# Performance work log

Measured on AMD Instinct MI355X. Metric: run time of the kernel, lower is better.

The kernel has to match this reference:

```python
import jax, jax.numpy as jnp
import numpy as np

N_NODES = 50000
NEG_SLOPE = 0.2


def _gat_conv(x, src, dst, W, a_src, a_dst, b, num_nodes):
    # W: [H*C, F_in]; a_src/a_dst: [H, C]; b: [H*C]
    H, C = a_src.shape
    xp = (x @ W.T).reshape(num_nodes, H, C)              # [N,H,C]
    alpha_s = jnp.sum(xp * a_src[None], axis=-1)          # [N,H]
    alpha_d = jnp.sum(xp * a_dst[None], axis=-1)          # [N,H]
    e = jax.nn.leaky_relu(alpha_s[src] + alpha_d[dst], NEG_SLOPE)  # [E,H]
    # segment softmax over incoming edges of each dst node (self-loops guarantee non-empty segments)
    m = jax.ops.segment_max(e, dst, num_segments=num_nodes)
    e = jnp.exp(e - m[dst])
    s = jax.ops.segment_sum(e, dst, num_segments=num_nodes)
    alpha = e / s[dst]                                    # [E,H]
    out = jax.ops.segment_sum(alpha[:, :, None] * xp[src], dst, num_segments=num_nodes)  # [N,H,C]
    return out.reshape(num_nodes, H * C) + b


def setup_inputs() -> dict:
    key = jax.random.key(0)
    ks = jax.random.split(key, 12)
    N, E, F_in, HID, H, Z = N_NODES, 800000, 128, 64, 2, 32
    sc = 0.1
    return {
        "features": jax.random.normal(ks[0], (N, F_in), jnp.float32),
        "edges": jax.random.randint(ks[1], (2, E), 0, N, jnp.int32),
        "W1": jax.random.normal(ks[2], (H * HID, F_in), jnp.float32) * sc,
        "a_src1": jax.random.normal(ks[3], (H, HID), jnp.float32) * sc,
        "a_dst1": jax.random.normal(ks[4], (H, HID), jnp.float32) * sc,
        "b1": jnp.zeros((H * HID,), jnp.float32),
        "W_mu": jax.random.normal(ks[5], (Z, H * HID), jnp.float32) * sc,
        "a_src_mu": jax.random.normal(ks[6], (1, Z), jnp.float32) * sc,
        "a_dst_mu": jax.random.normal(ks[7], (1, Z), jnp.float32) * sc,
        "b_mu": jnp.zeros((Z,), jnp.float32),
        "W_std": jax.random.normal(ks[8], (Z, H * HID), jnp.float32) * sc,
        "a_src_std": jax.random.normal(ks[9], (1, Z), jnp.float32) * sc,
        "a_dst_std": jax.random.normal(ks[10], (1, Z), jnp.float32) * sc,
        "b_std": jnp.zeros((Z,), jnp.float32),
    }


def reference(features, edges, W1, a_src1, a_dst1, b1, W_mu, a_src_mu, a_dst_mu, b_mu, W_std, a_src_std, a_dst_std, b_std):
    N = features.shape[0]
    loops = jnp.arange(N, dtype=edges.dtype)
    src = jnp.concatenate([edges[0], loops])  # add self loops (PyG default)
    dst = jnp.concatenate([edges[1], loops])
    h = _gat_conv(features, src, dst, W1, a_src1, a_dst1, b1, N)
    h = jax.nn.relu(h)  # dropout p=0.0 -> identity
    mu = _gat_conv(h, src, dst, W_mu, a_src_mu, a_dst_mu, b_mu, N)
    std = _gat_conv(h, src, dst, W_std, a_src_std, a_dst_std, b_std, N)
    return (mu, std)
```

## Files before the change

### kernel.cpp

```cpp
#include <hip/hip_runtime.h>
#include <math.h>

#define N_NODES 50000
#define N_EDGES 800000
#define ET (N_EDGES + N_NODES)
#define KD 128
#define Z 32
#define SH 7
#define BW 128
#define NBUCK ((N_NODES + BW - 1) / BW)
#define CHUNK 4096
#define NBLKA ((ET + CHUNK - 1) / CHUNK)
#define MTOT (NBUCK * NBLKA)
#define MBS ((MTOT + 1023) / 1024)

typedef __attribute__((ext_vector_type(8))) short bf16x8;
typedef __attribute__((ext_vector_type(4))) float f32x4;

static __device__ __forceinline__ float lrelu(float x){ return x > 0.f ? x : 0.2f*x; }
static __device__ __forceinline__ float bf2f(unsigned int u16){ return __uint_as_float(u16 << 16); }
static __device__ __forceinline__ float lof(unsigned int u){ return __uint_as_float(u << 16); }
static __device__ __forceinline__ float hif(unsigned int u){ return __uint_as_float(u & 0xffff0000u); }
static __device__ __forceinline__ unsigned short f2bf(float f){
  unsigned int x = __float_as_uint(f);
  return (unsigned short)((x + 0x7fffu + ((x >> 16) & 1u)) >> 16);
}

__global__ __launch_bounds__(256) void bhistA_kernel(const int* __restrict__ edges, int* __restrict__ M){
  int k = blockIdx.x, t = threadIdx.x;
  __shared__ int cnt[NBUCK];
  for(int b = t; b < NBUCK; b += 256) cnt[b] = 0;
  __syncthreads();
  int base = k*CHUNK;
  int lim = min(base + CHUNK, ET);
  for(int i = base + t; i < lim; i += 256){
    int d = (i < N_EDGES) ? edges[N_EDGES + i] : (i - N_EDGES);
    atomicAdd(&cnt[d >> SH], 1);
  }
  __syncthreads();
  for(int b = t; b < NBUCK; b += 256) M[b*NBLKA + k] = cnt[b];
}

__global__ __launch_bounds__(256) void scanM1_kernel(const int* __restrict__ M, int* __restrict__ bsumM){
  int b = blockIdx.x, t = threadIdx.x;
  int base = b*1024 + t*4;
  int s = 0;
  #pragma unroll
  for(int i=0;i<4;i++){ int n = base+i; if(n < MTOT) s += M[n]; }
  for(int off=32; off; off>>=1) s += __shfl_xor(s, off);
  __shared__ int ws[4];
  if((t&63)==0) ws[t>>6] = s;
  __syncthreads();
  if(t==0) bsumM[b] = ws[0]+ws[1]+ws[2]+ws[3];
}

__global__ __launch_bounds__(256) void scanM2_kernel(const int* __restrict__ bsumM, int* __restrict__ bpreM){
  __shared__ int sm[256];
  int t = threadIdx.x;
  int v = (t < MBS) ? bsumM[t] : 0;
  sm[t] = v;
  __syncthreads();
  for(int off=1; off<256; off<<=1){
    int u = (t >= off) ? sm[t-off] : 0;
    __syncthreads();
    sm[t] += u;
    __syncthreads();
  }
  if(t < MBS) bpreM[t] = sm[t] - v;
}

__global__ __launch_bounds__(256) void scanM3_kernel(const int* __restrict__ M, const int* __restrict__ bpreM,
                                                     int* __restrict__ Mpos){
  int b = blockIdx.x, t = threadIdx.x;
  int lane = t & 63, wv = t >> 6;
  int base = b*1024 + t*4;
  int d[4]; int s = 0;
  #pragma unroll
  for(int i=0;i<4;i++){ int n = base+i; d[i] = (n < MTOT) ? M[n] : 0; s += d[i]; }
  int v = s;
  for(int off=1; off<64; off<<=1){
    int u = __shfl_up(v, off);
    if(lane >= off) v += u;
  }
  int texcl = v - s;
  __shared__ int wtot[4];
  if(lane == 63) wtot[wv] = v;
  __syncthreads();
  int woff = 0;
  for(int i=0;i<wv;i++) woff += wtot[i];
  int run = bpreM[b] + woff + texcl;
  #pragma unroll
  for(int i=0;i<4;i++){
    int n = base+i;
    if(n < MTOT){ Mpos[n] = run; run += d[i]; }
  }
}

__global__ __launch_bounds__(256) void bplaceA_kernel(const int* __restrict__ edges, const int* __restrict__ Mpos,
                                                      int2* __restrict__ etmp){
  int k = blockIdx.x, t = threadIdx.x;
  __shared__ int cur[NBUCK];
  for(int b = t; b < NBUCK; b += 256) cur[b] = Mpos[b*NBLKA + k];
  __syncthreads();
  int base = k*CHUNK;
  int lim = min(base + CHUNK, ET);
  for(int i = base + t; i < lim; i += 256){
    int s, d;
    if(i < N_EDGES){ s = edges[i]; d = edges[N_EDGES+i]; } else { s = d = i - N_EDGES; }
    int pos = atomicAdd(&cur[d >> SH], 1);
    etmp[pos] = make_int2(s, d);
  }
}

__global__ __launch_bounds__(256) void bfin_kernel(const int* __restrict__ Mpos, const int2* __restrict__ etmp,
                                                   int* __restrict__ rowptr, int* __restrict__ esrc,
                                                   int* __restrict__ edst){
  int b = blockIdx.x, t = threadIdx.x;
  __shared__ int cnt[BW];
  __shared__ int pre[BW];
  __shared__ int lcur[BW];
  if(t < BW) cnt[t] = 0;
  __syncthreads();
  int beg = Mpos[b*NBLKA];
  int end = (b+1 < NBUCK) ? Mpos[(b+1)*NBLKA] : ET;
  for(int i = beg + t; i < end; i += 256) atomicAdd(&cnt[etmp[i].y & (BW-1)], 1);
  __syncthreads();
  if(t < BW) pre[t] = cnt[t];
  __syncthreads();
  for(int off=1; off<BW; off<<=1){
    int u = 0;
    if(t < BW && t >= off) u = pre[t-off];
    __syncthreads();
    if(t < BW) pre[t] += u;
    __syncthreads();
  }
  if(t < BW){
    int excl = pre[t] - cnt[t];
    int node = b*BW + t;
    if(node < N_NODES) rowptr[node] = beg + excl;
    lcur[t] = beg + excl;
  }
  if(b == 0 && t == 255) rowptr[N_NODES] = ET;
  __syncthreads();
  for(int i = beg + t; i < end; i += 256){
    int2 e = etmp[i];
    int pos = atomicAdd(&lcur[e.y & (BW-1)], 1);
    esrc[pos] = e.x;
    edst[pos] = e.y;
  }
}

__global__ __launch_bounds__(256) void wconv_kernel(const float* __restrict__ W1,
                                                    const float* __restrict__ Wmu, const float* __restrict__ Wst,
                                                    unsigned short* __restrict__ Wb1, unsigned short* __restrict__ Wb2){
  int i = blockIdx.x*256 + threadIdx.x;
  if(i < 128*KD) Wb1[i] = f2bf(W1[i]);
  if(i < 64*KD) Wb2[i] = f2bf(i < 32*KD ? Wmu[i] : Wst[i - 32*KD]);
}

__global__ __launch_bounds__(256) void mmt1_kernel(const float* __restrict__ X,
                                                   const unsigned short* __restrict__ Wb,
                                                   const float* __restrict__ asv, const float* __restrict__ adv,
                                                   unsigned short* __restrict__ outb,
                                                   float* __restrict__ as1, float* __restrict__ ad1){
  constexpr int OC = 128, CT = 8;
  int t = threadIdx.x;
  int w = t >> 6, L = t & 63;
  int col = L & 15, quad = L >> 4;
  int row0 = blockIdx.x*64 + w*16;
  int rA = row0 + col;
  if(rA >= N_NODES) rA = N_NODES-1;

  f32x4 acc[CT];
  #pragma unroll
  for(int ct=0;ct<CT;ct++) acc[ct] = (f32x4){0.f,0.f,0.f,0.f};

  #pragma unroll
  for(int kc=0;kc<4;kc++){
    int k0 = kc*32 + quad*8;
    const float* Xf = X + (size_t)rA*KD + k0;
    float4 p = *(const float4*)Xf;
    float4 q = *(const float4*)(Xf + 4);
    bf16x8 a;
    a[0] = (short)f2bf(p.x); a[1] = (short)f2bf(p.y);
    a[2] = (short)f2bf(p.z); a[3] = (short)f2bf(p.w);
    a[4] = (short)f2bf(q.x); a[5] = (short)f2bf(q.y);
    a[6] = (short)f2bf(q.z); a[7] = (short)f2bf(q.w);
    #pragma unroll
    for(int ct=0;ct<CT;ct++){
      bf16x8 b = *(const bf16x8*)(Wb + (size_t)(ct*16 + col)*KD + k0);
      acc[ct] = __builtin_amdgcn_mfma_f32_16x16x32_bf16(a, b, acc[ct], 0, 0, 0);
    }
  }

  float av[CT], dv[CT];
  #pragma unroll
  for(int ct=0;ct<CT;ct++){ av[ct] = asv[ct*16 + col]; dv[ct] = adv[ct*16 + col]; }

  #pragma unroll
  for(int r=0;r<4;r++){
    int row = row0 + quad*4 + r;
    #pragma unroll
    for(int ct=0;ct<CT;ct++)
      if(row < N_NODES) outb[(size_t)row*OC + ct*16 + col] = f2bf(acc[ct][r]);
    float s0 = acc[0][r]*av[0] + acc[1][r]*av[1] + acc[2][r]*av[2] + acc[3][r]*av[3];
    float s1 = acc[4][r]*av[4] + acc[5][r]*av[5] + acc[6][r]*av[6] + acc[7][r]*av[7];
    float d0 = acc[0][r]*dv[0] + acc[1][r]*dv[1] + acc[2][r]*dv[2] + acc[3][r]*dv[3];
    float d1 = acc[4][r]*dv[4] + acc[5][r]*dv[5] + acc[6][r]*dv[6] + acc[7][r]*dv[7];
    #pragma unroll
    for(int off=1; off<16; off<<=1){
      s0 += __shfl_xor(s0, off); s1 += __shfl_xor(s1, off);
      d0 += __shfl_xor(d0, off); d1 += __shfl_xor(d1, off);
    }
    if(col == 0 && row < N_NODES){
      as1[row*2] = s0; as1[row*2+1] = s1;
      ad1[row*2] = d0; ad1[row*2+1] = d1;
    }
  }
}

__global__ __launch_bounds__(256) void mmt2_kernel(const unsigned short* __restrict__ Xb,
                                                   const unsigned short* __restrict__ Wb,
                                                   const float* __restrict__ asmu, const float* __restrict__ admu,
                                                   const float* __restrict__ asst, const float* __restrict__ adst,
                                                   unsigned short* __restrict__ outb,
                                                   float* __restrict__ as2, float* __restrict__ ad2){
  constexpr int OC = 64, CT = 4;
  int t = threadIdx.x;
  int w = t >> 6, L = t & 63;
  int col = L & 15, quad = L >> 4;
  int row0 = blockIdx.x*64 + w*16;
  int rA = row0 + col;
  if(rA >= N_NODES) rA = N_NODES-1;

  f32x4 acc[CT];
  #pragma unroll
  for(int ct=0;ct<CT;ct++) acc[ct] = (f32x4){0.f,0.f,0.f,0.f};

  #pragma unroll
  for(int kc=0;kc<4;kc++){
    int k0 = kc*32 + quad*8;
    bf16x8 a = *(const bf16x8*)(Xb + (size_t)rA*KD + k0);
    #pragma unroll
    for(int ct=0;ct<CT;ct++){
      bf16x8 b = *(const bf16x8*)(Wb + (size_t)(ct*16 + col)*KD + k0);
      acc[ct] = __builtin_amdgcn_mfma_f32_16x16x32_bf16(a, b, acc[ct], 0, 0, 0);
    }
  }

  float av[CT], dv[CT];
  #pragma unroll
  for(int ct=0;ct<CT;ct++){
    av[ct] = (ct < 2) ? asmu[ct*16 + col] : asst[(ct-2)*16 + col];
    dv[ct] = (ct < 2) ? admu[ct*16 + col] : adst[(ct-2)*16 + col];
  }

  #pragma unroll
  for(int r=0;r<4;r++){
    int row = row0 + quad*4 + r;
    #pragma unroll
    for(int ct=0;ct<CT;ct++)
      if(row < N_NODES) outb[(size_t)row*OC + ct*16 + col] = f2bf(acc[ct][r]);
    float smu = acc[0][r]*av[0] + acc[1][r]*av[1];
    float sst = acc[2][r]*av[2] + acc[3][r]*av[3];
    float dmu = acc[0][r]*dv[0] + acc[1][r]*dv[1];
    float dst = acc[2][r]*dv[2] + acc[3][r]*dv[3];
    #pragma unroll
    for(int off=1; off<16; off<<=1){
      smu += __shfl_xor(smu, off); sst += __shfl_xor(sst, off);
      dmu += __shfl_xor(dmu, off); dst += __shfl_xor(dst, off);
    }
    if(col == 0 && row < N_NODES){
      as2[row*2] = smu; as2[row*2+1] = sst;
      ad2[row*2] = dmu; ad2[row*2+1] = dst;
    }
  }
}

__global__ __launch_bounds__(256) void wcalc_kernel(const int* __restrict__ esrc, const int* __restrict__ edst,
                                                    const float* __restrict__ as, const float* __restrict__ ad,
                                                    float2* __restrict__ wp){
  int i = blockIdx.x*256 + threadIdx.x;
  if(i >= ET) return;
  int s = esrc[i], d = edst[i];
  float2 a = ((const float2*)as)[s];
  float2 b = ((const float2*)ad)[d];
  wp[i] = make_float2(__expf(lrelu(a.x + b.x)), __expf(lrelu(a.y + b.y)));
}

__global__ __launch_bounds__(256) void agg1_kernel(const int* __restrict__ rowptr, const int* __restrict__ esrc,
                                                   const float2* __restrict__ wp,
                                                   const unsigned int* __restrict__ xb,
                                                   const float* __restrict__ b1, unsigned int* __restrict__ hb){
  int node = blockIdx.x*4 + (threadIdx.x>>6);
  int l = threadIdx.x & 63;
  if(node >= N_NODES) return;
  int beg = rowptr[node], end = rowptr[node+1];
  float accx = 0.f, accy = 0.f, s0 = 0.f, s1 = 0.f;
  int n = end - beg;
  int nq = n & ~7;

#define F1_E(j)  int e##j = esrc[i+j];
#define F1_W(j)  float2 w##j = wp[i+j];
#define F1_U(j)  unsigned int u##j = xb[(size_t)e##j*64 + l];
#define F1_C(j)  { s0 += w##j.x; s1 += w##j.y; \
                   float vv = (l < 32) ? w##j.x : w##j.y; \
                   accx += vv * lof(u##j); accy += vv * hif(u##j); }

  for(int i = beg; i < beg + nq; i += 8){
    F1_E(0) F1_E(1) F1_E(2) F1_E(3) F1_E(4) F1_E(5) F1_E(6) F1_E(7)
    F1_W(0) F1_W(1) F1_W(2) F1_W(3) F1_W(4) F1_W(5) F1_W(6) F1_W(7)
    F1_U(0) F1_U(1) F1_U(2) F1_U(3) F1_U(4) F1_U(5) F1_U(6) F1_U(7)
    F1_C(0) F1_C(1) F1_C(2) F1_C(3) F1_C(4) F1_C(5) F1_C(6) F1_C(7)
  }
  for(int i = beg + nq; i < end; i++){
    F1_E(0) F1_W(0) F1_U(0) F1_C(0)
  }
#undef F1_E
#undef F1_W
#undef F1_U
#undef F1_C
  float sd = (l < 32) ? s0 : s1;
  float2 bb = ((const float2*)b1)[l];
  float rx = fmaxf(accx/sd + bb.x, 0.f);
  float ry = fmaxf(accy/sd + bb.y, 0.f);
  unsigned int hp = (unsigned int)f2bf(rx) | ((unsigned int)f2bf(ry) << 16);
  hb[(size_t)node*64 + l] = hp;
}

__global__ __launch_bounds__(256) void agg2_kernel(const int* __restrict__ rowptr, const int* __restrict__ esrc,
                                                   const float2* __restrict__ wp,
                                                   const uint2* __restrict__ xb2,
                                                   const float* __restrict__ bmu, const float* __restrict__ bst,
                                                   float* __restrict__ out){
  int node = blockIdx.x*4 + (threadIdx.x>>6);
  int l = threadIdx.x & 63;
  if(node >= N_NODES) return;
  int g = l >> 4, c = l & 15;
  int beg = rowptr[node], end = rowptr[node+1];
  int n = end - beg;
  float a0=0.f, a1=0.f, a2=0.f, a3=0.f, smu=0.f, sst=0.f;
  int nquad = n >> 2;
  int mainq = nquad & ~3;

#define G2(j) int e##j = esrc[base + 4*j]; float2 w##j = wp[base + 4*j];
#define U2(j) uint2 u##j = xb2[(size_t)e##j*16 + c];
#define C2(j) { smu += w##j.x; sst += w##j.y; \
                float vv = (c < 8) ? w##j.x : w##j.y; \
                a0 += vv*lof(u##j.x); a1 += vv*hif(u##j.x); \
                a2 += vv*lof(u##j.y); a3 += vv*hif(u##j.y); }

  for(int qq = 0; qq < mainq; qq += 4){
    int base = beg + 4*qq + g;
    G2(0) G2(1) G2(2) G2(3)
    U2(0) U2(1) U2(2) U2(3)
    C2(0) C2(1) C2(2) C2(3)
  }
  for(int qq = mainq; qq < nquad; qq++){
    int base = beg + 4*qq + g;
    G2(0) U2(0) C2(0)
  }
  int tail = n & 3;
  if(g < tail){
    int idx = beg + 4*nquad + g;
    int e = esrc[idx];
    float2 w = wp[idx];
    uint2 u = xb2[(size_t)e*16 + c];
    smu += w.x; sst += w.y;
    float vv = (c < 8) ? w.x : w.y;
    a0 += vv*lof(u.x); a1 += vv*hif(u.x);
    a2 += vv*lof(u.y); a3 += vv*hif(u.y);
  }
#undef G2
#undef U2
#undef C2
  #pragma unroll
  for(int off = 16; off < 64; off <<= 1){
    smu += __shfl_xor(smu, off); sst += __shfl_xor(sst, off);
    a0 += __shfl_xor(a0, off); a1 += __shfl_xor(a1, off);
    a2 += __shfl_xor(a2, off); a3 += __shfl_xor(a3, off);
  }
  float sd = (c < 8) ? smu : sst;
  float4 bb = (c < 8) ? *(const float4*)(bmu + 4*c) : *(const float4*)(bst + 4*(c-8));
  float4 r;
  r.x = a0/sd + bb.x;
  r.y = a1/sd + bb.y;
  r.z = a2/sd + bb.z;
  r.w = a3/sd + bb.w;
  if(g == 0){
    float* dst = (c < 8) ? (out + (size_t)node*Z + 4*c)
                         : (out + (size_t)N_NODES*Z + (size_t)node*Z + 4*(c-8));
    *(float4*)dst = r;
  }
}

extern "C" void kernel_launch(void* const* d_in, const int* in_sizes, int n_in,
                              void* d_out, int out_size, void* d_ws, size_t ws_size,
                              hipStream_t stream){
  const float* x    = (const float*)d_in[0];
  const int*   edges= (const int*)d_in[1];
  const float* W1   = (const float*)d_in[2];
  const float* as1v = (const float*)d_in[3];
  const float* ad1v = (const float*)d_in[4];
  const float* b1   = (const float*)d_in[5];
  const float* Wmu  = (const float*)d_in[6];
  const float* asmu = (const float*)d_in[7];
  const float* admu = (const float*)d_in[8];
  const float* bmu  = (const float*)d_in[9];
  const float* Wst  = (const float*)d_in[10];
  const float* asst = (const float*)d_in[11];
  const float* adst = (const float*)d_in[12];
  const float* bst  = (const float*)d_in[13];
  float* out = (float*)d_out;

  char* p = (char*)d_ws;
  auto alloc = [&](size_t bytes)->char*{ char* r = p; p += (bytes + 255) & ~size_t(255); return r; };
  int*   M      = (int*)  alloc((size_t)MTOT*4);
  int*   Mpos   = (int*)  alloc((size_t)MTOT*4);
  int*   bsumM  = (int*)  alloc((size_t)MBS*4);
  int*   bpreM  = (int*)  alloc((size_t)MBS*4);
  int2*  etmp   = (int2*) alloc((size_t)ET*8);
  int*   esrc   = (int*)  alloc((size_t)ET*4);
  int*   edst   = (int*)  alloc((size_t)ET*4);
  int*   rowptr = (int*)  alloc((size_t)(N_NODES+1)*4);
  unsigned short* Wb1 = (unsigned short*)alloc((size_t)128*KD*2);
  unsigned short* Wb2 = (unsigned short*)alloc((size_t)64*KD*2);
  unsigned short* xpb1 = (unsigned short*)alloc((size_t)N_NODES*128*2);
  float* as1    = (float*)alloc((size_t)N_NODES*2*4);
  float* ad1    = (float*)alloc((size_t)N_NODES*2*4);
  unsigned short* hb = (unsigned short*)alloc((size_t)N_NODES*128*2);
  float* as2    = (float*)alloc((size_t)N_NODES*2*4);
  float* ad2    = (float*)alloc((size_t)N_NODES*2*4);
  unsigned short* xpb2 = xpb1;
  float2* wedge = (float2*)etmp;

  bhistA_kernel  <<<NBLKA, 256, 0, stream>>>(edges, M);
  scanM1_kernel  <<<MBS, 256, 0, stream>>>(M, bsumM);
  scanM2_kernel  <<<1, 256, 0, stream>>>(bsumM, bpreM);
  scanM3_kernel  <<<MBS, 256, 0, stream>>>(M, bpreM, Mpos);
  bplaceA_kernel <<<NBLKA, 256, 0, stream>>>(edges, Mpos, etmp);
  bfin_kernel    <<<NBUCK, 256, 0, stream>>>(Mpos, etmp, rowptr, esrc, edst);

  wconv_kernel   <<<(128*KD + 255)/256, 256, 0, stream>>>(W1, Wmu, Wst, Wb1, Wb2);

  mmt1_kernel  <<<(N_NODES+63)/64, 256, 0, stream>>>(x, Wb1, as1v, ad1v, xpb1, as1, ad1);
  wcalc_kernel <<<(ET+255)/256, 256, 0, stream>>>(esrc, edst, as1, ad1, wedge);
  agg1_kernel  <<<(N_NODES+3)/4, 256, 0, stream>>>(rowptr, esrc, wedge, (const unsigned int*)xpb1, b1, (unsigned int*)hb);

  mmt2_kernel  <<<(N_NODES+63)/64, 256, 0, stream>>>(hb, Wb2, asmu, admu, asst, adst, xpb1, as2, ad2);
  wcalc_kernel <<<(ET+255)/256, 256, 0, stream>>>(esrc, edst, as2, ad2, wedge);
  agg2_kernel  <<<(N_NODES+3)/4, 256, 0, stream>>>(rowptr, esrc, wedge, (const uint2*)xpb2, bmu, bst, out);
}
```

Before: 252.9 us.

## Widen aggregation gathers to 16-byte loads with multi-edge lanes per wave

Both aggregation kernels now gather source features with uint4 loads, so each lane holds 8 bf16 channels and several lane groups handle different edges in parallel. Partial sums are combined with xor shuffles across groups. The tail is handled by masked speculative loads, and esrc is padded by 32 zeroed entries so reads past the end stay in bounds. The goal is fewer, wider memory transactions and more edges in flight per wave, at the cost of extra shuffle reductions and wasted lanes on low-degree nodes.

```diff
diff --git a/kernel.cpp b/kernel.cpp
--- a/kernel.cpp
+++ b/kernel.cpp
@@ -18,12 +18,14 @@
 typedef __attribute__((ext_vector_type(4))) float f32x4;
 
 static __device__ __forceinline__ float lrelu(float x){ return x > 0.f ? x : 0.2f*x; }
-static __device__ __forceinline__ float bf2f(unsigned int u16){ return __uint_as_float(u16 << 16); }
 static __device__ __forceinline__ float lof(unsigned int u){ return __uint_as_float(u << 16); }
 static __device__ __forceinline__ float hif(unsigned int u){ return __uint_as_float(u & 0xffff0000u); }
 static __device__ __forceinline__ unsigned short f2bf(float f){
   unsigned int x = __float_as_uint(f);
   return (unsigned short)((x + 0x7fffu + ((x >> 16) & 1u)) >> 16);
+}
+static __device__ __forceinline__ unsigned int pack2(float lo, float hi){
+  return (unsigned int)f2bf(lo) | ((unsigned int)f2bf(hi) << 16);
 }
 
 __global__ __launch_bounds__(256) void bhistA_kernel(const int* __restrict__ edges, int* __restrict__ M){
@@ -120,6 +122,7 @@
   __shared__ int pre[BW];
   __shared__ int lcur[BW];
   if(t < BW) cnt[t] = 0;
+  if(b == 0 && t < 32) esrc[ET + t] = 0;
   __syncthreads();
   int beg = Mpos[b*NBLKA];
   int end = (b+1 < NBUCK) ? Mpos[(b+1)*NBLKA] : ET;
@@ -290,107 +293,156 @@
 
 __global__ __launch_bounds__(256) void agg1_kernel(const int* __restrict__ rowptr, const int* __restrict__ esrc,
                                                    const float2* __restrict__ wp,
-                                                   const unsigned int* __restrict__ xb,
-                                                   const float* __restrict__ b1, unsigned int* __restrict__ hb){
-  int node = blockIdx.x*4 + (threadIdx.x>>6);
-  int l = threadIdx.x & 63;
-  if(node >= N_NODES) return;
-  int beg = rowptr[node], end = rowptr[node+1];
-  float accx = 0.f, accy = 0.f, s0 = 0.f, s1 = 0.f;
-  int n = end - beg;
-  int nq = n & ~7;
-
-#define F1_E(j)  int e##j = esrc[i+j];
-#define F1_W(j)  float2 w##j = wp[i+j];
-#define F1_U(j)  unsigned int u##j = xb[(size_t)e##j*64 + l];
-#define F1_C(j)  { s0 += w##j.x; s1 += w##j.y; \
-                   float vv = (l < 32) ? w##j.x : w##j.y; \
-                   accx += vv * lof(u##j); accy += vv * hif(u##j); }
-
-  for(int i = beg; i < beg + nq; i += 8){
-    F1_E(0) F1_E(1) F1_E(2) F1_E(3) F1_E(4) F1_E(5) F1_E(6) F1_E(7)
-    F1_W(0) F1_W(1) F1_W(2) F1_W(3) F1_W(4) F1_W(5) F1_W(6) F1_W(7)
-    F1_U(0) F1_U(1) F1_U(2) F1_U(3) F1_U(4) F1_U(5) F1_U(6) F1_U(7)
-    F1_C(0) F1_C(1) F1_C(2) F1_C(3) F1_C(4) F1_C(5) F1_C(6) F1_C(7)
-  }
-  for(int i = beg + nq; i < end; i++){
-    F1_E(0) F1_W(0) F1_U(0) F1_C(0)
-  }
-#undef F1_E
-#undef F1_W
-#undef F1_U
-#undef F1_C
-  float sd = (l < 32) ? s0 : s1;
-  float2 bb = ((const float2*)b1)[l];
-  float rx = fmaxf(accx/sd + bb.x, 0.f);
-  float ry = fmaxf(accy/sd + bb.y, 0.f);
-  unsigned int hp = (unsigned int)f2bf(rx) | ((unsigned int)f2bf(ry) << 16);
-  hb[(size_t)node*64 + l] = hp;
-}
-
-__global__ __launch_bounds__(256) void agg2_kernel(const int* __restrict__ rowptr, const int* __restrict__ esrc,
-                                                   const float2* __restrict__ wp,
-                                                   const uint2* __restrict__ xb2,
-                                                   const float* __restrict__ bmu, const float* __restrict__ bst,
-                                                   float* __restrict__ out){
+                                                   const uint4* __restrict__ xb4,
+                                                   const float* __restrict__ b1, uint4* __restrict__ hb4){
   int node = blockIdx.x*4 + (threadIdx.x>>6);
   int l = threadIdx.x & 63;
   if(node >= N_NODES) return;
   int g = l >> 4, c = l & 15;
   int beg = rowptr[node], end = rowptr[node+1];
   int n = end - beg;
-  float a0=0.f, a1=0.f, a2=0.f, a3=0.f, smu=0.f, sst=0.f;
-  int nquad = n >> 2;
-  int mainq = nquad & ~3;
-
-#define G2(j) int e##j = esrc[base + 4*j]; float2 w##j = wp[base + 4*j];
-#define U2(j) uint2 u##j = xb2[(size_t)e##j*16 + c];
-#define C2(j) { smu += w##j.x; sst += w##j.y; \
-                float vv = (c < 8) ? w##j.x : w##j.y; \
-                a0 += vv*lof(u##j.x); a1 += vv*hif(u##j.x); \
-                a2 += vv*lof(u##j.y); a3 += vv*hif(u##j.y); }
-
-  for(int qq = 0; qq < mainq; qq += 4){
-    int base = beg + 4*qq + g;
-    G2(0) G2(1) G2(2) G2(3)
-    U2(0) U2(1) U2(2) U2(3)
-    C2(0) C2(1) C2(2) C2(3)
-  }
-  for(int qq = mainq; qq < nquad; qq++){
-    int base = beg + 4*qq + g;
-    G2(0) U2(0) C2(0)
-  }
-  int tail = n & 3;
-  if(g < tail){
-    int idx = beg + 4*nquad + g;
-    int e = esrc[idx];
-    float2 w = wp[idx];
-    uint2 u = xb2[(size_t)e*16 + c];
-    smu += w.x; sst += w.y;
-    float vv = (c < 8) ? w.x : w.y;
-    a0 += vv*lof(u.x); a1 += vv*hif(u.x);
-    a2 += vv*lof(u.y); a3 += vv*hif(u.y);
-  }
-#undef G2
-#undef U2
-#undef C2
-  #pragma unroll
-  for(int off = 16; off < 64; off <<= 1){
-    smu += __shfl_xor(smu, off); sst += __shfl_xor(sst, off);
-    a0 += __shfl_xor(a0, off); a1 += __shfl_xor(a1, off);
-    a2 += __shfl_xor(a2, off); a3 += __shfl_xor(a3, off);
-  }
-  float sd = (c < 8) ? smu : sst;
-  float4 bb = (c < 8) ? *(const float4*)(bmu + 4*c) : *(const float4*)(bst + 4*(c-8));
-  float4 r;
-  r.x = a0/sd + bb.x;
-  r.y = a1/sd + bb.y;
-  r.z = a2/sd + bb.z;
-  r.w = a3/sd + bb.w;
+  float a0=0.f,a1=0.f,a2=0.f,a3=0.f,a4=0.f,a5=0.f,a6=0.f,a7=0.f;
+  float s0=0.f, s1=0.f;
+
+#define S1_STEP(IDX) { \
+    int e_ = esrc[(IDX)]; \
+    float2 w_ = wp[(IDX)]; \
+    uint4 u_ = xb4[(size_t)e_*16 + c]; \
+    s0 += w_.x; s1 += w_.y; \
+    float vv = (c < 8) ? w_.x : w_.y; \
+    a0 += vv*lof(u_.x); a1 += vv*hif(u_.x); \
+    a2 += vv*lof(u_.y); a3 += vv*hif(u_.y); \
+    a4 += vv*lof(u_.z); a5 += vv*hif(u_.z); \
+    a6 += vv*lof(u_.w); a7 += vv*hif(u_.w); }
+
+#define S1_STEPM(IDX) { \
+    int e_ = esrc[(IDX)]; \
+    float2 w_ = wp[(IDX)]; \
+    uint4 u_ = xb4[(size_t)e_*16 + c]; \
+    float wx_ = ((IDX) < end) ? w_.x : 0.f; \
+    float wy_ = ((IDX) < end) ? w_.y : 0.f; \
+    s0 += wx_; s1 += wy_; \
+    float vv = (c < 8) ? wx_ : wy_; \
+    a0 += vv*lof(u_.x); a1 += vv*hif(u_.x); \
+    a2 += vv*lof(u_.y); a3 += vv*hif(u_.y); \
+    a4 += vv*lof(u_.z); a5 += vv*hif(u_.z); \
+    a6 += vv*lof(u_.w); a7 += vv*hif(u_.w); }
+
+  int i = beg;
+  int nfull = n & ~7;
+  for(; i < beg + nfull; i += 8){
+    S1_STEP(i + g)
+    S1_STEP(i + 4 + g)
+  }
+  if(i < end){
+    S1_STEPM(i + g)
+    S1_STEPM(i + 4 + g)
+  }
+#undef S1_STEP
+#undef S1_STEPM
+
+  #pragma unroll
+  for(int off=16; off<64; off<<=1){
+    s0 += __shfl_xor(s0,off); s1 += __shfl_xor(s1,off);
+    a0 += __shfl_xor(a0,off); a1 += __shfl_xor(a1,off);
+    a2 += __shfl_xor(a2,off); a3 += __shfl_xor(a3,off);
+    a4 += __shfl_xor(a4,off); a5 += __shfl_xor(a5,off);
+    a6 += __shfl_xor(a6,off); a7 += __shfl_xor(a7,off);
+  }
   if(g == 0){
-    float* dst = (c < 8) ? (out + (size_t)node*Z + 4*c)
-                         : (out + (size_t)N_NODES*Z + (size_t)node*Z + 4*(c-8));
-    *(float4*)dst = r;
+    float sd = (c < 8) ? s0 : s1;
+    float inv = 1.f / sd;
+    const float4* bp = (const float4*)(b1 + 8*c);
+    float4 bl = bp[0], bh = bp[1];
+    float r0 = fmaxf(a0*inv + bl.x, 0.f);
+    float r1 = fmaxf(a1*inv + bl.y, 0.f);
+    float r2 = fmaxf(a2*inv + bl.z, 0.f);
+    float r3 = fmaxf(a3*inv + bl.w, 0.f);
+    float r4 = fmaxf(a4*inv + bh.x, 0.f);
+    float r5 = fmaxf(a5*inv + bh.y, 0.f);
+    float r6 = fmaxf(a6*inv + bh.z, 0.f);
+    float r7 = fmaxf(a7*inv + bh.w, 0.f);
+    uint4 o;
+    o.x = pack2(r0, r1); o.y = pack2(r2, r3);
+    o.z = pack2(r4, r5); o.w = pack2(r6, r7);
+    hb4[(size_t)node*16 + c] = o;
+  }
+}
+
+__global__ __launch_bounds__(256) void agg2_kernel(const int* __restrict__ rowptr, const int* __restrict__ esrc,
+                                                   const float2* __restrict__ wp,
+                                                   const uint4* __restrict__ xb4,
+                                                   const float* __restrict__ bmu, const float* __restrict__ bst,
+                                                   float* __restrict__ out){
+  int node = blockIdx.x*4 + (threadIdx.x>>6);
+  int l = threadIdx.x & 63;
+  if(node >= N_NODES) return;
+  int g = l >> 3, c = l & 7;
+  int beg = rowptr[node], end = rowptr[node+1];
+  int n = end - beg;
+  float a0=0.f,a1=0.f,a2=0.f,a3=0.f,a4=0.f,a5=0.f,a6=0.f,a7=0.f;
+  float smu=0.f, sst=0.f;
+
+#define S2_STEP(IDX) { \
+    int e_ = esrc[(IDX)]; \
+    float2 w_ = wp[(IDX)]; \
+    uint4 u_ = xb4[(size_t)e_*8 + c]; \
+    smu += w_.x; sst += w_.y; \
+    float vv = (c < 4) ? w_.x : w_.y; \
+    a0 += vv*lof(u_.x); a1 += vv*hif(u_.x); \
+    a2 += vv*lof(u_.y); a3 += vv*hif(u_.y); \
+    a4 += vv*lof(u_.z); a5 += vv*hif(u_.z); \
+    a6 += vv*lof(u_.w); a7 += vv*hif(u_.w); }
+
+#define S2_STEPM(IDX) { \
+    int e_ = esrc[(IDX)]; \
+    float2 w_ = wp[(IDX)]; \
+    uint4 u_ = xb4[(size_t)e_*8 + c]; \
+    float wx_ = ((IDX) < end) ? w_.x : 0.f; \
+    float wy_ = ((IDX) < end) ? w_.y : 0.f; \
+    smu += wx_; sst += wy_; \
+    float vv = (c < 4) ? wx_ : wy_; \
+    a0 += vv*lof(u_.x); a1 += vv*hif(u_.x); \
+    a2 += vv*lof(u_.y); a3 += vv*hif(u_.y); \
+    a4 += vv*lof(u_.z); a5 += vv*hif(u_.z); \
+    a6 += vv*lof(u_.w); a7 += vv*hif(u_.w); }
+
+  int i = beg;
+  int nfull = n & ~15;
+  for(; i < beg + nfull; i += 16){
+    S2_STEP(i + g)
+    S2_STEP(i + 8 + g)
+  }
+  if(i < end){
+    S2_STEPM(i + g)
+    S2_STEPM(i + 8 + g)
+  }
+#undef S2_STEP
+#undef S2_STEPM
+
+  #pragma unroll
+  for(int off=8; off<64; off<<=1){
+    smu += __shfl_xor(smu,off); sst += __shfl_xor(sst,off);
+    a0 += __shfl_xor(a0,off); a1 += __shfl_xor(a1,off);
+    a2 += __shfl_xor(a2,off); a3 += __shfl_xor(a3,off);
+    a4 += __shfl_xor(a4,off); a5 += __shfl_xor(a5,off);
+    a6 += __shfl_xor(a6,off); a7 += __shfl_xor(a7,off);
+  }
+  if(g == 0){
+    float sd = (c < 4) ? smu : sst;
+    float inv = 1.f / sd;
+    const float* bb = (c < 4) ? (bmu + 8*c) : (bst + 8*(c-4));
+    float4 bl = *(const float4*)bb;
+    float4 bh = *(const float4*)(bb + 4);
+    float* op = (c < 4) ? (out + (size_t)node*Z + 8*c)
+                        : (out + (size_t)N_NODES*Z + (size_t)node*Z + 8*(c-4));
+    float4 r0, r1;
+    r0.x = a0*inv + bl.x; r0.y = a1*inv + bl.y;
+    r0.z = a2*inv + bl.z; r0.w = a3*inv + bl.w;
+    r1.x = a4*inv + bh.x; r1.y = a5*inv + bh.y;
+    r1.z = a6*inv + bh.z; r1.w = a7*inv + bh.w;
+    *(float4*)op = r0;
+    *((float4*)op + 1) = r1;
   }
 }
 
@@ -419,8 +471,8 @@
   int*   Mpos   = (int*)  alloc((size_t)MTOT*4);
   int*   bsumM  = (int*)  alloc((size_t)MBS*4);
   int*   bpreM  = (int*)  alloc((size_t)MBS*4);
-  int2*  etmp   = (int2*) alloc((size_t)ET*8);
-  int*   esrc   = (int*)  alloc((size_t)ET*4);
+  int2*  etmp   = (int2*) alloc((size_t)(ET+32)*8);
+  int*   esrc   = (int*)  alloc((size_t)(ET+32)*4);
   int*   edst   = (int*)  alloc((size_t)ET*4);
   int*   rowptr = (int*)  alloc((size_t)(N_NODES+1)*4);
   unsigned short* Wb1 = (unsigned short*)alloc((size_t)128*KD*2);
@@ -445,9 +497,9 @@
 
   mmt1_kernel  <<<(N_NODES+63)/64, 256, 0, stream>>>(x, Wb1, as1v, ad1v, xpb1, as1, ad1);
   wcalc_kernel <<<(ET+255)/256, 256, 0, stream>>>(esrc, edst, as1, ad1, wedge);
-  agg1_kernel  <<<(N_NODES+3)/4, 256, 0, stream>>>(rowptr, esrc, wedge, (const unsigned int*)xpb1, b1, (unsigned int*)hb);
+  agg1_kernel  <<<(N_NODES+3)/4, 256, 0, stream>>>(rowptr, esrc, wedge, (const uint4*)xpb1, b1, (uint4*)hb);
 
   mmt2_kernel  <<<(N_NODES+63)/64, 256, 0, stream>>>(hb, Wb2, asmu, admu, asst, adst, xpb1, as2, ad2);
   wcalc_kernel <<<(ET+255)/256, 256, 0, stream>>>(esrc, edst, as2, ad2, wedge);
-  agg2_kernel  <<<(N_NODES+3)/4, 256, 0, stream>>>(rowptr, esrc, wedge, (const uint2*)xpb2, bmu, bst, out);
-}
+  agg2_kernel  <<<(N_NODES+3)/4, 256, 0, stream>>>(rowptr, esrc, wedge, (const uint4*)xpb2, bmu, bst, out);
+}
```

Measured after the change: 238.8 us. -5.6%, faster.
